# Performance work log

Hardware: AMD Instinct MI355X
Metric: run time of the kernel (lower is better)

## Reference

```python
import jax, jax.numpy as jnp
import numpy as np
from jax import lax

TAU = 2.0
V_TH = 1.0
ALPHA = 4.0   # spikingjelly surrogate.Sigmoid default
BN_EPS = 1e-5
HEADS = 8


def lif(x):
    """Multi-step LIF neuron (tau=2, v_reset=0, hard reset, detach_reset).
    x: [T, ...] -> spikes [T, ...]. Forward is Heaviside; sigmoid surrogate
    is wired in via straight-through for the bwd variant."""
    def step(v, xt):
        v = v + (xt - v) / TAU                      # charge
        sg = jax.nn.sigmoid(ALPHA * (v - V_TH))     # surrogate
        hard = (v >= V_TH).astype(x.dtype)
        spike = sg + lax.stop_gradient(hard - sg)   # fwd: hard, bwd: sigmoid'
        v = v * (1.0 - lax.stop_gradient(spike))    # detached hard reset to 0
        return v, spike
    _, s = lax.scan(step, jnp.zeros_like(x[0]), x)
    return s


def conv1x1_bn(x, w, g, b, m, var, bias=None):
    # x: [N, C, H, W]; 1x1 conv == channel matmul, then eval-mode BN
    y = jnp.einsum('nchw,dc->ndhw', x, w)
    if bias is not None:
        y = y + bias[None, :, None, None]
    scale = g / jnp.sqrt(var + BN_EPS)
    shift = b - m * scale
    return y * scale[None, :, None, None] + shift[None, :, None, None]


def to_heads(x, T, B, C, H, W):
    # [T,B,C,H,W] -> [T,B,heads,N,hd]
    N = H * W
    hd = C // HEADS
    x = x.reshape(T, B, C, N).transpose(0, 1, 3, 2)          # [T,B,N,C]
    return x.reshape(T, B, N, HEADS, hd).transpose(0, 1, 3, 2, 4)


def _forward(x, q_w, q_bn_g, q_bn_b, q_bn_m, q_bn_v,
             k_w, k_bn_g, k_bn_b, k_bn_m, k_bn_v,
             v_w, v_bn_g, v_bn_b, v_bn_m, v_bn_v,
             out_w, out_b, out_bn_g, out_bn_b, out_bn_m, out_bn_v):
    T, B, C, H, W = x.shape
    N = H * W
    identity = x

    xs = lif(x)                                  # shortcut_lif
    x_qkv = xs.reshape(T * B, C, H, W)

    q = lif(conv1x1_bn(x_qkv, q_w, q_bn_g, q_bn_b, q_bn_m, q_bn_v).reshape(T, B, C, H, W))
    k = lif(conv1x1_bn(x_qkv, k_w, k_bn_g, k_bn_b, k_bn_m, k_bn_v).reshape(T, B, C, H, W))
    v = lif(conv1x1_bn(x_qkv, v_w, v_bn_g, v_bn_b, v_bn_m, v_bn_v).reshape(T, B, C, H, W))

    qh = to_heads(q, T, B, C, H, W)              # [T,B,h,N,hd]
    kh = to_heads(k, T, B, C, H, W)
    vh = to_heads(v, T, B, C, H, W)

    kv = jnp.sum(kh * vh, axis=-2, keepdims=True)   # [T,B,h,1,hd]
    kv = lif(kv)                                    # talking_heads_proj_lif
    y = qh * kv                                     # [T,B,h,N,hd]

    # [T,B,h,N,hd] -> transpose(3,4) -> [T,B,h,hd,N] -> [T,B,C,H,W]
    y = y.transpose(0, 1, 2, 4, 3).reshape(T, B, C, H, W)
    y = conv1x1_bn(y.reshape(T * B, C, H, W), out_w, out_bn_g, out_bn_b,
                   out_bn_m, out_bn_v, bias=out_b).reshape(T, B, C, H, W)
    return y + identity, vh


def setup_inputs() -> dict:
    key = jax.random.key(0)
    ks = jax.random.split(key, 6)
    T, B, C, H, W = 4, 32, 512, 14, 14
    inp = {
        'x': jax.random.normal(ks[0], (T, B, C, H, W), dtype=jnp.float32),
        'q_w': jax.random.normal(ks[1], (C, C), dtype=jnp.float32) * 0.05,
        'k_w': jax.random.normal(ks[2], (C, C), dtype=jnp.float32) * 0.05,
        'v_w': jax.random.normal(ks[3], (C, C), dtype=jnp.float32) * 0.05,
        'out_w': jax.random.normal(ks[4], (C, C), dtype=jnp.float32) * 0.05,
        'out_b': jnp.zeros((C,), dtype=jnp.float32),
    }
    for p in ('q', 'k', 'v', 'out'):
        inp[f'{p}_bn_g'] = jnp.ones((C,), dtype=jnp.float32)
        inp[f'{p}_bn_b'] = jnp.zeros((C,), dtype=jnp.float32)
        inp[f'{p}_bn_m'] = jnp.zeros((C,), dtype=jnp.float32)
        inp[f'{p}_bn_v'] = jnp.ones((C,), dtype=jnp.float32)
    return inp


def reference(x, q_w, q_bn_g, q_bn_b, q_bn_m, q_bn_v,
              k_w, k_bn_g, k_bn_b, k_bn_m, k_bn_v,
              v_w, v_bn_g, v_bn_b, v_bn_m, v_bn_v,
              out_w, out_b, out_bn_g, out_bn_b, out_bn_m, out_bn_v):
    return _forward(x, q_w, q_bn_g, q_bn_b, q_bn_m, q_bn_v,
                    k_w, k_bn_g, k_bn_b, k_bn_m, k_bn_v,
                    v_w, v_bn_g, v_bn_b, v_bn_m, v_bn_v,
                    out_w, out_b, out_bn_g, out_bn_b, out_bn_m, out_bn_v)
```

## Files before the change

kernel.cpp:

```cpp
#include <hip/hip_runtime.h>
#include <math.h>

#define T_   4
#define B_   32
#define C_   512
#define N_   196
#define TB_  128
#define M_   25088
#define BNP_ 6272
#define OUT1_ 12845056

typedef unsigned short ushort_t;
typedef __attribute__((ext_vector_type(8)))  __bf16 bf16x8;
typedef __attribute__((ext_vector_type(16))) float  f32x16;

__device__ __forceinline__ ushort_t f2bf(float f) {
    unsigned int u = __float_as_uint(f);
    u = u + 0x7FFFu + ((u >> 16) & 1u);
    return (ushort_t)(u >> 16);
}
__device__ __forceinline__ float bf2f(ushort_t h) {
    return __uint_as_float(((unsigned int)h) << 16);
}

#define GL2LDS(gp, lp) \
    __builtin_amdgcn_global_load_lds((const __attribute__((address_space(1))) void*)(gp), \
                                     (__attribute__((address_space(3))) void*)(lp), 16, 0, 0)

__global__ void prep_kernel(
    const float* __restrict__ qw, const float* __restrict__ kw,
    const float* __restrict__ vw, const float* __restrict__ ow,
    const float* __restrict__ qg, const float* __restrict__ qb, const float* __restrict__ qm, const float* __restrict__ qv,
    const float* __restrict__ kg, const float* __restrict__ kb, const float* __restrict__ km, const float* __restrict__ kvr,
    const float* __restrict__ vg, const float* __restrict__ vb, const float* __restrict__ vm, const float* __restrict__ vv,
    const float* __restrict__ og, const float* __restrict__ ob, const float* __restrict__ om, const float* __restrict__ ov,
    const float* __restrict__ obias,
    ushort_t* __restrict__ wsplit, ushort_t* __restrict__ osplit,
    float* __restrict__ scale_qkv, float* __restrict__ shift_qkv,
    float* __restrict__ scale_o,   float* __restrict__ shift_o,
    float* __restrict__ kvpart)
{
    int i = blockIdx.x * 256 + threadIdx.x;
    int d = i >> 9, c = i & 511;
    const float* src = (d < 512) ? qw : (d < 1024) ? kw : vw;
    float wv = src[(d & 511) * 512 + c];
    ushort_t h = f2bf(wv);
    float r1 = wv - bf2f(h);
    ushort_t mm = f2bf(r1);
    wsplit[((size_t)d * 2 + 0) * 512 + c] = h;
    wsplit[((size_t)d * 2 + 1) * 512 + c] = mm;
    if (d < 512)
        osplit[(size_t)d * 512 + c] = f2bf(ow[d * 512 + c]);

    if (i < 3 * C_) {
        int p = i >> 9, dl = i & 511;
        const float* g = (p == 0) ? qg : (p == 1) ? kg : vg;
        const float* b = (p == 0) ? qb : (p == 1) ? kb : vb;
        const float* m = (p == 0) ? qm : (p == 1) ? km : vm;
        const float* r = (p == 0) ? qv : (p == 1) ? kvr : vv;
        float sc = g[dl] / sqrtf(r[dl] + 1e-5f);
        scale_qkv[i] = sc;
        shift_qkv[i] = b[dl] - m[dl] * sc;
    }
    if (i < C_) {
        float sc = og[i] / sqrtf(ov[i] + 1e-5f);
        scale_o[i] = sc;
        shift_o[i] = ob[i] - om[i] * sc + obias[i] * sc;
    }
    if (i < TB_ * C_) kvpart[i] = 0.f;
}

__global__ __launch_bounds__(256)
void lifx_kernel(const float* __restrict__ x, ushort_t* __restrict__ xs)
{
    __shared__ ushort_t tile[64 * 66];
    const int tid = threadIdx.x;
    const int b = blockIdx.z, c0 = blockIdx.y * 64, n0 = blockIdx.x * 64;
    const int j = tid & 63, w = tid >> 6;
    const bool nok = (n0 + j) < N_;
    float v[16];
#pragma unroll
    for (int r = 0; r < 16; ++r) v[r] = 0.f;
    for (int t = 0; t < T_; ++t) {
        const float* xb = x + ((size_t)((t * B_ + b) * C_ + c0)) * N_ + n0 + j;
#pragma unroll
        for (int r = 0; r < 16; ++r) {
            int i = w * 16 + r;
            float xv = nok ? xb[(size_t)i * N_] : 0.f;
            v[r] = v[r] + (xv - v[r]) * 0.5f;
            bool s = (v[r] >= 1.0f);
            tile[j * 66 + i] = s ? 0x3F80 : 0;
            if (s) v[r] = 0.f;
        }
        __syncthreads();
#pragma unroll
        for (int p = 0; p < 2; ++p) {
            int w2 = tid + p * 256;
            int jj = w2 >> 3, ck = w2 & 7;
            if (n0 + jj < N_) {
                const unsigned int* src = reinterpret_cast<const unsigned int*>(&tile[jj * 66 + ck * 8]);
                uint4 dv; dv.x = src[0]; dv.y = src[1]; dv.z = src[2]; dv.w = src[3];
                size_t mp = (size_t)(b * N_ + n0 + jj) * 4 + t;
                *reinterpret_cast<uint4*>(&xs[mp * 512 + c0 + ck * 8]) = dv;
            }
        }
        __syncthreads();
    }
}

__global__ __launch_bounds__(256, 2)
void qkv_gemm_lif(const ushort_t* __restrict__ W, const ushort_t* __restrict__ X,
                  const float* __restrict__ scale, const float* __restrict__ shift,
                  ushort_t* __restrict__ spk, float* __restrict__ out2)
{
    const int id = blockIdx.x;
    const int xw = id & 7, local = id >> 3;
    const int ml = local / 12, d_t = local - ml * 12;
    const int m_t = ml * 8 + xw;
    if (m_t >= 98) return;
    const int m0 = m_t * 256;
    const int d0 = d_t * 128;

    __shared__ ushort_t Xs[16 * 512];
    __shared__ ushort_t Ws[16 * 512];
    const int tid = threadIdx.x, wid = tid >> 6, lane = tid & 63;
    const int mw = (wid & 1) * 128, dw = (wid >> 1) * 64;
    const int row32 = lane & 31, khalf = lane >> 5;

    f32x16 acc[4][2] = {};

    for (int k0 = 0; k0 < 512; k0 += 32) {
        __syncthreads();
        for (int q = wid; q < 16; q += 4) {
            int mb = q >> 1, ks = q & 1;
            const ushort_t* g = X + (size_t)(m0 + mb * 32 + row32) * 512 + k0 + ks * 16 + khalf * 8;
            GL2LDS(g, &Xs[q * 512]);
        }
        for (int q = wid; q < 16; q += 4) {
            int s = q >> 3, rem = q & 7, db = rem >> 1, ks = rem & 1;
            const ushort_t* g = W + ((size_t)(d0 + db * 32 + row32) * 2 + s) * 512 + k0 + ks * 16 + khalf * 8;
            GL2LDS(g, &Ws[q * 512]);
        }
        __syncthreads();

#pragma unroll
        for (int ks = 0; ks < 2; ++ks) {
            bf16x8 xfr[4];
#pragma unroll
            for (int i = 0; i < 4; ++i)
                xfr[i] = *reinterpret_cast<const bf16x8*>(&Xs[(((mw >> 5) + i) * 2 + ks) * 512 + lane * 8]);
#pragma unroll
            for (int s = 0; s < 2; ++s)
#pragma unroll
                for (int j = 0; j < 2; ++j) {
                    bf16x8 wfr = *reinterpret_cast<const bf16x8*>(
                        &Ws[(s * 8 + ((dw >> 5) + j) * 2 + ks) * 512 + lane * 8]);
#pragma unroll
                    for (int i = 0; i < 4; ++i)
                        acc[i][j] = __builtin_amdgcn_mfma_f32_32x32x16_bf16(xfr[i], wfr, acc[i][j], 0, 0, 0);
                }
        }
    }

    const int p = d0 >> 9;
    const bool isV = (p == 2);
    ushort_t* plane = spk + (size_t)p * ((size_t)M_ * 512);
#pragma unroll
    for (int j = 0; j < 2; ++j) {
        int d = d0 + dw + j * 32 + row32;
        float sc = scale[d], sh = shift[d];
        int dl = d & 511;
        int h = dl >> 6, hd = dl & 63;
#pragma unroll
    for (int i = 0; i < 4; ++i) {
            int bnb = (m0 + mw + i * 32) >> 2;
            f32x16 a = acc[i][j];
#pragma unroll
            for (int g = 0; g < 4; ++g) {
                int bn = bnb + 2 * g + khalf;
                float p0 = fmaf(a[4 * g + 0], sc, sh);
                float p1 = fmaf(a[4 * g + 1], sc, sh);
                float p2 = fmaf(a[4 * g + 2], sc, sh);
                float p3 = fmaf(a[4 * g + 3], sc, sh);
                float v = p0 * 0.5f;
                bool s0 = (v >= 1.f); if (s0) v = 0.f;
                v = v + (p1 - v) * 0.5f;
                bool s1 = (v >= 1.f); if (s1) v = 0.f;
                v = v + (p2 - v) * 0.5f;
                bool s2 = (v >= 1.f); if (s2) v = 0.f;
                v = v + (p3 - v) * 0.5f;
                bool s3 = (v >= 1.f);
                ushort_t* b0 = plane + (size_t)bn * 512 + dl;
                b0[0]                      = s0 ? 0x3F80 : 0;
                b0[(size_t)BNP_ * 512]     = s1 ? 0x3F80 : 0;
                b0[(size_t)2 * BNP_ * 512] = s2 ? 0x3F80 : 0;
                b0[(size_t)3 * BNP_ * 512] = s3 ? 0x3F80 : 0;
                if (isV) {
                    int b = bn / N_, n = bn - b * N_;
                    float* o = out2 + (((size_t)b * 8 + h) * N_ + n) * 64 + hd;
                    o[0]                       = s0 ? 1.f : 0.f;
                    o[(size_t)1 * (OUT1_ / 4)] = s1 ? 1.f : 0.f;
                    o[(size_t)2 * (OUT1_ / 4)] = s2 ? 1.f : 0.f;
                    o[(size_t)3 * (OUT1_ / 4)] = s3 ? 1.f : 0.f;
                }
            }
        }
    }
}

__global__ void kv_part_kernel(const ushort_t* __restrict__ ks, const ushort_t* __restrict__ vs,
                               float* __restrict__ kvpart)
{
    int id = blockIdx.x;
    int tb = id >> 3, r = id & 7;
    int c  = (r & 1) * 256 + threadIdx.x;
    int n0 = (r >> 1) * 49;
    const ushort_t* kb = ks + (size_t)tb * N_ * 512 + c;
    const ushort_t* vb = vs + (size_t)tb * N_ * 512 + c;
    int cnt = 0;
    for (int n = n0; n < n0 + 49; ++n)
        cnt += (kb[(size_t)n * 512] & vb[(size_t)n * 512]) ? 1 : 0;
    atomicAdd(&kvpart[tb * 512 + c], (float)cnt);
}

__global__ void kv_lif_kernel(const float* __restrict__ kvpart, ushort_t* __restrict__ kvs)
{
    int i = blockIdx.x * 256 + threadIdx.x;
    if (i >= B_ * C_) return;
    int b = i >> 9, c = i & 511;
    float v = 0.f;
#pragma unroll
    for (int t = 0; t < T_; ++t) {
        float y = kvpart[((t * B_ + b) << 9) + c];
        v = v + (y - v) * 0.5f;
        bool s = (v >= 1.f);
        kvs[((t * B_ + b) << 9) + c] = s ? 0x3F80 : 0;
        if (s) v = 0.f;
    }
}

__global__ __launch_bounds__(256)
void out_gemm(const ushort_t* __restrict__ A, const ushort_t* __restrict__ qs,
              const ushort_t* __restrict__ kvs,
              const float* __restrict__ scale, const float* __restrict__ shift,
              const float* __restrict__ xid, float* __restrict__ out)
{
    const int id = blockIdx.x;
    const int xw = id & 7, local = id >> 3;
    const int m_t = (local >> 2) * 8 + xw, d_t = local & 3;
    if (m_t >= 196) return;
    const int m0 = m_t * 128, d0 = d_t * 128;

    __shared__ ushort_t As[8 * 512];
    __shared__ ushort_t Bs[8 * 512];
    const int tid = threadIdx.x, wid = tid >> 6, lane = tid & 63;
    const int dw = (wid >> 1) * 64, mw = (wid & 1) * 64;
    const int row32 = lane & 31, khalf = lane >> 5;

    int sm[2], stb[2], sq[2], sL[2];
#pragma unroll
    for (int u = 0; u < 2; ++u) {
        int s = tid + u * 256;
        sq[u] = s >> 6; sL[u] = s & 63;
        sm[u] = m0 + (sq[u] >> 1) * 32 + (sL[u] & 31);
        stb[u] = sm[u] / N_;
    }

    f32x16 acc[2][2] = {};

    for (int k0 = 0; k0 < 512; k0 += 32) {
        __syncthreads();
        for (int q = wid; q < 8; q += 4) {
            int db = q >> 1, ks = q & 1;
            const ushort_t* g = A + (size_t)(d0 + db * 32 + row32) * 512 + k0 + ks * 16 + khalf * 8;
            GL2LDS(g, &As[q * 512]);
        }
#pragma unroll
        for (int u = 0; u < 2; ++u) {
            int kk = k0 + (sq[u] & 1) * 16 + (sL[u] >> 5) * 8;
            uint4 qv = *reinterpret_cast<const uint4*>(&qs[(size_t)sm[u] * 512 + kk]);
            uint4 kv = *reinterpret_cast<const uint4*>(&kvs[(size_t)stb[u] * 512 + kk]);
            uint4 o; o.x = qv.x & kv.x; o.y = qv.y & kv.y; o.z = qv.z & kv.z; o.w = qv.w & kv.w;
            *reinterpret_cast<uint4*>(&Bs[sq[u] * 512 + sL[u] * 8]) = o;
        }
        __syncthreads();

#pragma unroll
        for (int ks = 0; ks < 2; ++ks) {
            bf16x8 afr[2];
#pragma unroll
            for (int i = 0; i < 2; ++i)
                afr[i] = *reinterpret_cast<const bf16x8*>(&As[(((dw >> 5) + i) * 2 + ks) * 512 + lane * 8]);
#pragma unroll
            for (int j = 0; j < 2; ++j) {
                bf16x8 bfr = *reinterpret_cast<const bf16x8*>(&Bs[(((mw >> 5) + j) * 2 + ks) * 512 + lane * 8]);
#pragma unroll
                for (int i = 0; i < 2; ++i)
                    acc[i][j] = __builtin_amdgcn_mfma_f32_32x32x16_bf16(afr[i], bfr, acc[i][j], 0, 0, 0);
            }
        }
    }

#pragma unroll
    for (int j = 0; j < 2; ++j) {
        int m = m0 + mw + j * 32 + row32;
        int tb = m / N_;
        int n  = m - tb * N_;
        size_t mbase = (size_t)tb * (C_ * N_) + n;
#pragma unroll
        for (int i = 0; i < 2; ++i) {
            int dbase = d0 + dw + i * 32 + 4 * khalf;
            f32x16 a = acc[i][j];
#pragma unroll
            for (int g = 0; g < 4; ++g) {
#pragma unroll
                for (int t = 0; t < 4; ++t) {
                    int d = dbase + t + 8 * g;
                    float val = fmaf(a[4 * g + t], scale[d], shift[d]);
                    size_t ad = mbase + (size_t)d * N_;
                    out[ad] = val + xid[ad];
                }
            }
        }
    }
}

extern "C" void kernel_launch(void* const* d_in, const int* in_sizes, int n_in,
                              void* d_out, int out_size, void* d_ws, size_t ws_size,
                              hipStream_t stream)
{
    const float* x    = (const float*)d_in[0];
    const float* q_w  = (const float*)d_in[1];
    const float* k_w  = (const float*)d_in[2];
    const float* v_w  = (const float*)d_in[3];
    const float* o_w  = (const float*)d_in[4];
    const float* o_b  = (const float*)d_in[5];
    const float* qg = (const float*)d_in[6],  *qb = (const float*)d_in[7],
               *qm = (const float*)d_in[8],  *qv = (const float*)d_in[9];
    const float* kg = (const float*)d_in[10], *kb = (const float*)d_in[11],
               *km = (const float*)d_in[12], *kv = (const float*)d_in[13];
    const float* vg = (const float*)d_in[14], *vb = (const float*)d_in[15],
               *vm = (const float*)d_in[16], *vv = (const float*)d_in[17];
    const float* og = (const float*)d_in[18], *ob = (const float*)d_in[19],
               *om = (const float*)d_in[20], *ov = (const float*)d_in[21];

    float* out1  = (float*)d_out;
    float* out2f = out1 + OUT1_;

    ushort_t* spk    = (ushort_t*)d_ws;
    ushort_t* xs     = spk + (size_t)3 * M_ * 512;
    ushort_t* wsplit = xs + (size_t)M_ * 512;
    ushort_t* osplit = wsplit + (size_t)1536 * 2 * 512;
    float*    kvpart = (float*)(osplit + (size_t)512 * 512);
    ushort_t* kvs    = (ushort_t*)(kvpart + TB_ * C_);
    float*    scq    = (float*)(kvs + TB_ * C_);
    float*    shq    = scq + 3 * C_;
    float*    sco    = shq + 3 * C_;
    float*    sho    = sco + C_;

    ushort_t* qsp = spk;
    ushort_t* ksp = spk + (size_t)M_ * 512;
    ushort_t* vsp = spk + (size_t)2 * M_ * 512;

    prep_kernel<<<(1536 * 512) / 256, 256, 0, stream>>>(
        q_w, k_w, v_w, o_w,
        qg, qb, qm, qv, kg, kb, km, kv, vg, vb, vm, vv, og, ob, om, ov, o_b,
        wsplit, osplit, scq, shq, sco, sho, kvpart);

    lifx_kernel<<<dim3(4, 8, 32), 256, 0, stream>>>(x, xs);

    qkv_gemm_lif<<<1200, 256, 0, stream>>>(wsplit, xs, scq, shq, spk, out2f);

    kv_part_kernel<<<1024, 256, 0, stream>>>(ksp, vsp, kvpart);

    kv_lif_kernel<<<64, 256, 0, stream>>>(kvpart, kvs);

    out_gemm<<<800, 256, 0, stream>>>(osplit, qsp, kvs, sco, sho, x, out1);
}
```

Before: 413.3 us.

## Double-buffer QKV GEMM LDS tiles and widen block to eight waves

Result: no change. 412.0 us (-0.3%).

```diff
diff --git a/kernel.cpp b/kernel.cpp
--- a/kernel.cpp
+++ b/kernel.cpp
@@ -108,7 +108,7 @@
     }
 }
 
-__global__ __launch_bounds__(256, 2)
+__global__ __launch_bounds__(512, 4)
 void qkv_gemm_lif(const ushort_t* __restrict__ W, const ushort_t* __restrict__ X,
                   const float* __restrict__ scale, const float* __restrict__ shift,
                   ushort_t* __restrict__ spk, float* __restrict__ out2)
@@ -121,45 +121,67 @@
     const int m0 = m_t * 256;
     const int d0 = d_t * 128;
 
-    __shared__ ushort_t Xs[16 * 512];
-    __shared__ ushort_t Ws[16 * 512];
+    __shared__ ushort_t Xs[2][16 * 512];
+    __shared__ ushort_t Ws[2][16 * 512];
     const int tid = threadIdx.x, wid = tid >> 6, lane = tid & 63;
-    const int mw = (wid & 1) * 128, dw = (wid >> 1) * 64;
+    const int mw = (wid & 3) * 64, dw = (wid >> 2) * 64;
     const int row32 = lane & 31, khalf = lane >> 5;
 
-    f32x16 acc[4][2] = {};
-
-    for (int k0 = 0; k0 < 512; k0 += 32) {
-        __syncthreads();
-        for (int q = wid; q < 16; q += 4) {
-            int mb = q >> 1, ks = q & 1;
+    f32x16 acc[2][2] = {};
+
+    auto STAGE = [&](int buf, int k0) {
+        {
+            int q = wid, mb = q >> 1, ks = q & 1;
             const ushort_t* g = X + (size_t)(m0 + mb * 32 + row32) * 512 + k0 + ks * 16 + khalf * 8;
-            GL2LDS(g, &Xs[q * 512]);
-        }
-        for (int q = wid; q < 16; q += 4) {
-            int s = q >> 3, rem = q & 7, db = rem >> 1, ks = rem & 1;
+            GL2LDS(g, &Xs[buf][q * 512]);
+        }
+        {
+            int q = wid + 8, mb = q >> 1, ks = q & 1;
+            const ushort_t* g = X + (size_t)(m0 + mb * 32 + row32) * 512 + k0 + ks * 16 + khalf * 8;
+            GL2LDS(g, &Xs[buf][q * 512]);
+        }
+        {
+            int q = wid, s = q >> 3, rem = q & 7, db = rem >> 1, ks = rem & 1;
             const ushort_t* g = W + ((size_t)(d0 + db * 32 + row32) * 2 + s) * 512 + k0 + ks * 16 + khalf * 8;
-            GL2LDS(g, &Ws[q * 512]);
-        }
-        __syncthreads();
-
+            GL2LDS(g, &Ws[buf][q * 512]);
+        }
+        {
+            int q = wid + 8, s = q >> 3, rem = q & 7, db = rem >> 1, ks = rem & 1;
+            const ushort_t* g = W + ((size_t)(d0 + db * 32 + row32) * 2 + s) * 512 + k0 + ks * 16 + khalf * 8;
+            GL2LDS(g, &Ws[buf][q * 512]);
+        }
+    };
+
+    STAGE(0, 0);
+    __syncthreads();
+    int cur = 0;
+
+    for (int it = 0; it < 16; ++it) {
+        if (it < 15) STAGE(cur ^ 1, (it + 1) * 32);
+
+        __builtin_amdgcn_s_setprio(1);
 #pragma unroll
         for (int ks = 0; ks < 2; ++ks) {
-            bf16x8 xfr[4];
-#pragma unroll
-            for (int i = 0; i < 4; ++i)
-                xfr[i] = *reinterpret_cast<const bf16x8*>(&Xs[(((mw >> 5) + i) * 2 + ks) * 512 + lane * 8]);
+            bf16x8 xfr[2];
+#pragma unroll
+            for (int i = 0; i < 2; ++i)
+                xfr[i] = *reinterpret_cast<const bf16x8*>(
+                    &Xs[cur][(((mw >> 5) + i) * 2 + ks) * 512 + lane * 8]);
 #pragma unroll
             for (int s = 0; s < 2; ++s)
 #pragma unroll
                 for (int j = 0; j < 2; ++j) {
                     bf16x8 wfr = *reinterpret_cast<const bf16x8*>(
-                        &Ws[(s * 8 + ((dw >> 5) + j) * 2 + ks) * 512 + lane * 8]);
-#pragma unroll
-                    for (int i = 0; i < 4; ++i)
+                        &Ws[cur][(s * 8 + ((dw >> 5) + j) * 2 + ks) * 512 + lane * 8]);
+#pragma unroll
+                    for (int i = 0; i < 2; ++i)
                         acc[i][j] = __builtin_amdgcn_mfma_f32_32x32x16_bf16(xfr[i], wfr, acc[i][j], 0, 0, 0);
                 }
         }
+        __builtin_amdgcn_s_setprio(0);
+
+        __syncthreads();
+        cur ^= 1;
     }
 
     const int p = d0 >> 9;
@@ -172,7 +194,7 @@
         int dl = d & 511;
         int h = dl >> 6, hd = dl & 63;
 #pragma unroll
-    for (int i = 0; i < 4; ++i) {
+        for (int i = 0; i < 2; ++i) {
             int bnb = (m0 + mw + i * 32) >> 2;
             f32x16 a = acc[i][j];
 #pragma unroll
@@ -369,7 +391,7 @@
 
     lifx_kernel<<<dim3(4, 8, 32), 256, 0, stream>>>(x, xs);
 
-    qkv_gemm_lif<<<1200, 256, 0, stream>>>(wsplit, xs, scq, shq, spk, out2f);
+    qkv_gemm_lif<<<1200, 512, 0, stream>>>(wsplit, xs, scq, shq, spk, out2f);
 
     kv_part_kernel<<<1024, 256, 0, stream>>>(ksp, vsp, kvpart);
 
```
